# Performance work log

Hardware: AMD Instinct MI355X
Metric: run time of the kernel (lower is better)

## Reference

```python
import jax, jax.numpy as jnp
import numpy as np
import math

B, T, D = 2, 2048, 1024
H, HKV = 16, 4
HD = D // H            # 64
G = H // HKV           # GQA group size = 4
ROPE_BASE = 10000.0


def _rope(x, cos, sin):
    # x: [B, T, h, HD]; rotate-half rotary embedding
    half = x.shape[-1] // 2
    x1, x2 = x[..., :half], x[..., half:]
    c = cos[None, :, None, :]  # [1,T,1,HD/2]
    s = sin[None, :, None, :]
    return jnp.concatenate([x1 * c - x2 * s, x1 * s + x2 * c], axis=-1)


def setup_inputs() -> dict:
    key = jax.random.key(0)
    ks = jax.random.split(key, 6)
    sD = 1.0 / math.sqrt(D)
    x = jax.random.normal(ks[0], (B, T, D), dtype=jnp.float32)
    Wq = jax.random.normal(ks[1], (D, D), dtype=jnp.float32) * sD
    Wk = jax.random.normal(ks[2], (HKV * HD, D), dtype=jnp.float32) * sD
    Wv = jax.random.normal(ks[3], (HKV * HD, D), dtype=jnp.float32) * sD
    Wp = jax.random.normal(ks[4], (D, D), dtype=jnp.float32) * sD
    q_gain = jnp.full((H,), 0.125, dtype=jnp.float32)  # qk_gain_init
    return {"x": x, "Wq": Wq, "Wk": Wk, "Wv": Wv, "Wp": Wp, "q_gain": q_gain}


def reference(x, Wq, Wk, Wv, Wp, q_gain):
    Bx, Tx, _ = x.shape
    # QKV projections (CastedLinear == plain no-bias linear in fp32 here)
    q = (x @ Wq.T).reshape(Bx, Tx, H, HD)
    k = (x @ Wk.T).reshape(Bx, Tx, HKV, HD)
    v = (x @ Wv.T).reshape(Bx, Tx, HKV, HD)

    # rotary tables
    inv_freq = 1.0 / (ROPE_BASE ** (jnp.arange(0, HD, 2, dtype=jnp.float32) / HD))
    freqs = jnp.arange(Tx, dtype=jnp.float32)[:, None] * inv_freq[None, :]  # [T, HD/2]
    cos, sin = jnp.cos(freqs), jnp.sin(freqs)

    q = _rope(q, cos, sin) * q_gain[None, None, :, None]  # per-head learned gain
    k = _rope(k, cos, sin)

    # grouped-query causal attention
    qg = q.reshape(Bx, Tx, HKV, G, HD)
    scale = 1.0 / math.sqrt(HD)
    scores = jnp.einsum('bqkgd,bskd->bkgqs', qg, k) * scale  # [B,HKV,G,T,T]
    causal = jnp.tril(jnp.ones((Tx, Tx), dtype=bool))
    scores = jnp.where(causal[None, None, None], scores, jnp.float32(-1e30))
    p = jax.nn.softmax(scores, axis=-1)
    o = jnp.einsum('bkgqs,bskd->bqkgd', p, v).reshape(Bx, Tx, D)
    return o @ Wp.T
```

## Files before the change

### kernel.cpp

```cpp
#include <hip/hip_runtime.h>

typedef unsigned short u16;
typedef unsigned int   u32;
typedef __bf16 bfv8 __attribute__((ext_vector_type(8)));
typedef float  f32x4 __attribute__((ext_vector_type(4)));
typedef short  s16x4 __attribute__((ext_vector_type(4)));

#define B_   2
#define T_   2048
#define D_   1024
#define H_   16
#define HKV_ 4
#define NQK  1280
#define BT_  (B_*T_)
#define QSCALE 0.18033688011112042f
#define L2_10K 0.41524101186092515f
#define I2PI   0.15915494309189535f

__device__ __forceinline__ u16 f2bf(float f) {
  __bf16 h = (__bf16)f; u16 s; __builtin_memcpy(&s, &h, 2); return s;
}

__device__ __forceinline__ void load16(const u16* g, u16* l) {
  auto gp = (const __attribute__((address_space(1))) u32*)(uintptr_t)g;
  auto lp = (__attribute__((address_space(3))) u32*)(uintptr_t)l;
  __builtin_amdgcn_global_load_lds(gp, lp, 16, 0, 0);
}

__device__ __forceinline__ void hw_sincos_rev(float rev, float& s, float& c) {
  rev -= floorf(rev);
  s = __builtin_amdgcn_sinf(rev);
  c = __builtin_amdgcn_cosf(rev);
}

__global__ void conv_all_kernel(const float* __restrict__ x,
                                const float* __restrict__ wq, const float* __restrict__ wk,
                                const float* __restrict__ wv, const float* __restrict__ wp,
                                u16* __restrict__ dst) {
  int i = (blockIdx.x * 256 + threadIdx.x) * 4;
  const float* s; int off;
  if (i < 4194304) { s = x; off = i; }
  else {
    int j = i - 4194304;
    if      (j < 1048576) { s = wq; off = j; }
    else if (j < 1310720) { s = wk; off = j - 1048576; }
    else if (j < 1572864) { s = wv; off = j - 1310720; }
    else                  { s = wp; off = j - 1572864; }
  }
  float4 v = *(const float4*)(s + off);
  ushort4 o; o.x = f2bf(v.x); o.y = f2bf(v.y); o.z = f2bf(v.z); o.w = f2bf(v.w);
  *(ushort4*)(dst + i) = o;
}

template<int MODE>
__global__ __launch_bounds__(256) void gemm_bt(const u16* __restrict__ A,
                                               const u16* __restrict__ Bm,
                                               void* __restrict__ C,
                                               u16* __restrict__ vT,
                                               const float* __restrict__ qg,
                                               int M, int N, int K) {
  __shared__ __align__(16) u16 As[2][128 * 32];
  __shared__ __align__(16) u16 Bs[2][128 * 32];
  const int tid  = threadIdx.x;
  const int wave = tid >> 6, lane = tid & 63;
  const int quad = lane >> 4, l16 = lane & 15;
  const int m0 = blockIdx.y * 128, n0 = blockIdx.x * 128;
  const int wm = (wave >> 1) * 64, wn = (wave & 1) * 64;
  const int lr = lane >> 2, lc = (lane & 3) * 8;

  f32x4 acc[4][4];
  for (int mi = 0; mi < 4; ++mi)
    for (int ni = 0; ni < 4; ++ni) acc[mi][ni] = (f32x4){0.f, 0.f, 0.f, 0.f};

  auto stage = [&](int kk, int buf) {
    #pragma unroll
    for (int u = 0; u < 2; ++u) {
      const int c = u * 4 + wave;
      load16(A + (size_t)(m0 + c*16 + lr) * K + kk + lc, As[buf] + c * 512);
    }
    #pragma unroll
    for (int u = 0; u < 2; ++u) {
      const int c = u * 4 + wave;
      load16(Bm + (size_t)(n0 + c*16 + lr) * K + kk + lc, Bs[buf] + c * 512);
    }
  };

  const int nIter = K >> 5;
  stage(0, 0);
  for (int it = 0; it < nIter; ++it) {
    __syncthreads();
    if (it + 1 < nIter) stage(((it + 1) << 5), (it + 1) & 1);
    const u16* Ab = As[it & 1];
    const u16* Bb = Bs[it & 1];
    bfv8 af[4], bf_[4];
    #pragma unroll
    for (int i = 0; i < 4; ++i) af[i]  = *(const bfv8*)(Ab + (wm + i*16 + l16)*32 + 8*quad);
    #pragma unroll
    for (int i = 0; i < 4; ++i) bf_[i] = *(const bfv8*)(Bb + (wn + i*16 + l16)*32 + 8*quad);
    #pragma unroll
    for (int mi = 0; mi < 4; ++mi)
      #pragma unroll
      for (int ni = 0; ni < 4; ++ni)
        acc[mi][ni] = __builtin_amdgcn_mfma_f32_16x16x32_bf16(af[mi], bf_[ni], acc[mi][ni], 0, 0, 0);
  }

  const int nc = n0 + wn;
  if (MODE == 0) {
    #pragma unroll
    for (int mi = 0; mi < 4; ++mi)
      #pragma unroll
      for (int ni = 0; ni < 4; ++ni)
        #pragma unroll
        for (int r = 0; r < 4; ++r)
          ((float*)C)[(size_t)(m0 + wm + mi*16 + 4*quad + r) * N + nc + ni*16 + l16]
            = acc[mi][ni][r];
  } else {
    if (nc < NQK) {
      const bool isQ = nc < 1024;
      const float gain = isQ ? qg[nc >> 6] * QSCALE : 1.0f;
      const float inv0 = exp2f(-(float)l16 * L2_10K) * I2PI;
      const float inv1 = exp2f(-(float)(l16 + 16) * L2_10K) * I2PI;
      #pragma unroll
      for (int mi = 0; mi < 4; ++mi) {
        const int rowg = m0 + wm + mi*16 + 4*quad;
        u16* dst = (u16*)C + (size_t)rowg * NQK + nc + l16;
        #pragma unroll
        for (int r = 0; r < 4; ++r) {
          const int t = (rowg + r) & (T_ - 1);
          float s0, c0, s1, c1;
          hw_sincos_rev((float)t * inv0, s0, c0);
          hw_sincos_rev((float)t * inv1, s1, c1);
          const float x1a = acc[mi][0][r], x2a = acc[mi][2][r];
          const float x1b = acc[mi][1][r], x2b = acc[mi][3][r];
          u16* drow = dst + (size_t)r * NQK;
          drow[0]  = f2bf((x1a*c0 - x2a*s0) * gain);
          drow[16] = f2bf((x1b*c1 - x2b*s1) * gain);
          drow[32] = f2bf((x1a*s0 + x2a*c0) * gain);
          drow[48] = f2bf((x1b*s1 + x2b*c1) * gain);
        }
      }
    } else {
      const int kvh = (nc - NQK) >> 6;
      #pragma unroll
      for (int mi = 0; mi < 4; ++mi)
        #pragma unroll
        for (int ni = 0; ni < 4; ++ni) {
          const int d = ni*16 + l16;
          const int rowg = m0 + wm + mi*16 + 4*quad;
          const int bb = rowg >> 11, t = rowg & (T_ - 1);
          ushort4 w4;
          w4.x = f2bf(acc[mi][ni][0]); w4.y = f2bf(acc[mi][ni][1]);
          w4.z = f2bf(acc[mi][ni][2]); w4.w = f2bf(acc[mi][ni][3]);
          *(ushort4*)(vT + ((size_t)((bb*HKV_ + kvh)*64 + d)) * T_ + t) = w4;
        }
    }
  }
}

template<bool DOA, bool DIAGA, bool DIAGB>
__device__ __forceinline__ void attn_tile(const u16* KB, const u16* VB,
                                          int l16, int quad,
                                          const bfv8* qA, const bfv8* qB,
                                          float& psA, float& psB,
                                          f32x4 oA[4], f32x4 oB[4],
                                          int qColA, int qColB, int s0) {
  const int sw = l16 & 7;
  f32x4 stA[4], stB[4];
  #pragma unroll
  for (int ni = 0; ni < 4; ++ni) {
    const int row = ni*16 + l16;
    bfv8 k0 = *(const bfv8*)(KB + row*64 + 8*(quad ^ sw));
    bfv8 k1 = *(const bfv8*)(KB + row*64 + 8*((quad + 4) ^ sw));
    if (DOA) {
      stA[ni] = __builtin_amdgcn_mfma_f32_16x16x32_bf16(k0, qA[0], (f32x4){0.f,0.f,0.f,0.f}, 0, 0, 0);
      stA[ni] = __builtin_amdgcn_mfma_f32_16x16x32_bf16(k1, qA[1], stA[ni], 0, 0, 0);
    }
    stB[ni] = __builtin_amdgcn_mfma_f32_16x16x32_bf16(k0, qB[0], (f32x4){0.f,0.f,0.f,0.f}, 0, 0, 0);
    stB[ni] = __builtin_amdgcn_mfma_f32_16x16x32_bf16(k1, qB[1], stB[ni], 0, 0, 0);
  }
  s16x4 pbA[4], pbB[4];
  #pragma unroll
  for (int ni = 0; ni < 4; ++ni)
    #pragma unroll
    for (int r = 0; r < 4; ++r) {
      const int key = s0 + ni*16 + 4*quad + r;
      if (DOA) {
        float v = stA[ni][r];
        if (DIAGA) v = (key <= qColA) ? v : -3.0e38f;
        const float p = __builtin_amdgcn_exp2f(v);
        psA += p;
        pbA[ni][r] = (short)f2bf(p);
      }
      float v = stB[ni][r];
      if (DIAGB) v = (key <= qColB) ? v : -3.0e38f;
      const float p = __builtin_amdgcn_exp2f(v);
      psB += p;
      pbB[ni][r] = (short)f2bf(p);
    }
  #pragma unroll
  for (int ni = 0; ni < 4; ++ni) {
    const int vofs = 8*((2*ni + (quad >> 1)) ^ sw) + 4*(quad & 1);
    #pragma unroll
    for (int dt = 0; dt < 4; ++dt) {
      s16x4 va = *(const s16x4*)(VB + (dt*16 + l16)*64 + vofs);
      if (DOA) oA[dt] = __builtin_amdgcn_mfma_f32_16x16x16bf16_1k(va, pbA[ni], oA[dt], 0, 0, 0);
      oB[dt] = __builtin_amdgcn_mfma_f32_16x16x16bf16_1k(va, pbB[ni], oB[dt], 0, 0, 0);
    }
  }
}

__global__ __launch_bounds__(256) void attn_kernel(const u16* __restrict__ qkv,
                                                   const u16* __restrict__ vT,
                                                   u16* __restrict__ o) {
  const int pr = blockIdx.x;
  const int h  = blockIdx.y;
  const int b  = blockIdx.z;
  const int kvh = h >> 2;
  const int tid = threadIdx.x;
  const int wave = tid >> 6, lane = tid & 63;
  const int quad = lane >> 4, l16 = lane & 15;

  const int qtA = pr, qtB = 31 - pr;
  const int nk  = qtB + 1;

  __shared__ __align__(16) u16 Kl[2][64 * 64];
  __shared__ __align__(16) u16 Vl[2][64 * 64];

  const u16* qAp = qkv + (size_t)(b*T_ + qtA*64 + wave*16 + l16) * NQK + h*64 + 8*quad;
  const u16* qBp = qkv + (size_t)(b*T_ + qtB*64 + wave*16 + l16) * NQK + h*64 + 8*quad;
  const bfv8 qA[2] = { *(const bfv8*)qAp, *(const bfv8*)(qAp + 32) };
  const bfv8 qB[2] = { *(const bfv8*)qBp, *(const bfv8*)(qBp + 32) };

  float psA = 0.f, psB = 0.f;
  f32x4 oA[4], oB[4];
  #pragma unroll
  for (int d = 0; d < 4; ++d) oA[d] = oB[d] = (f32x4){0.f, 0.f, 0.f, 0.f};

  const int srow = lane >> 3, slot = lane & 7;
  const u16* Kg = qkv + (size_t)(b*T_) * NQK + 1024 + kvh*64;
  const u16* Vg = vT  + (size_t)((b*HKV_ + kvh) * 64) * T_;

  auto stage = [&](int kt, int buf) {
    const int s0 = kt * 64;
    #pragma unroll
    for (int u = 0; u < 2; ++u) {
      const int base = wave*16 + u*8;
      const int r  = base + srow;
      const int kc = slot ^ (r & 7);
      load16(Kg + (size_t)(s0 + r) * NQK + kc*8, Kl[buf] + base*64);
      load16(Vg + (size_t)r * T_ + s0 + kc*8,    Vl[buf] + base*64);
    }
  };

  stage(0, 0);
  const int qColA = qtA*64 + wave*16 + l16;
  const int qColB = qtB*64 + wave*16 + l16;

  for (int kt = 0; kt < qtA; ++kt) {
    __syncthreads();
    stage(kt + 1, (kt + 1) & 1);
    attn_tile<true, false, false>(Kl[kt & 1], Vl[kt & 1], l16, quad, qA, qB,
                                  psA, psB, oA, oB, qColA, qColB, kt*64);
  }
  {
    const int kt = qtA;
    __syncthreads();
    stage(kt + 1, (kt + 1) & 1);
    attn_tile<true, true, false>(Kl[kt & 1], Vl[kt & 1], l16, quad, qA, qB,
                                 psA, psB, oA, oB, qColA, qColB, kt*64);
  }
  for (int kt = qtA + 1; kt < nk - 1; ++kt) {
    __syncthreads();
    stage(kt + 1, (kt + 1) & 1);
    attn_tile<false, false, false>(Kl[kt & 1], Vl[kt & 1], l16, quad, qA, qB,
                                   psA, psB, oA, oB, qColA, qColB, kt*64);
  }
  {
    const int kt = nk - 1;
    __syncthreads();
    attn_tile<false, false, true>(Kl[kt & 1], Vl[kt & 1], l16, quad, qA, qB,
                                  psA, psB, oA, oB, qColA, qColB, kt*64);
  }

  #pragma unroll
  for (int off = 16; off < 64; off <<= 1) {
    psA += __shfl_xor(psA, off);
    psB += __shfl_xor(psB, off);
  }
  const float ivA = 1.0f / psA, ivB = 1.0f / psB;

  #pragma unroll
  for (int dt = 0; dt < 4; ++dt) {
    ushort4 wA, wB;
    wA.x = f2bf(oA[dt][0]*ivA); wA.y = f2bf(oA[dt][1]*ivA);
    wA.z = f2bf(oA[dt][2]*ivA); wA.w = f2bf(oA[dt][3]*ivA);
    wB.x = f2bf(oB[dt][0]*ivB); wB.y = f2bf(oB[dt][1]*ivB);
    wB.z = f2bf(oB[dt][2]*ivB); wB.w = f2bf(oB[dt][3]*ivB);
    *(ushort4*)(o + (size_t)(b*T_ + qColA) * D_ + h*64 + dt*16 + 4*quad) = wA;
    *(ushort4*)(o + (size_t)(b*T_ + qColB) * D_ + h*64 + dt*16 + 4*quad) = wB;
  }
}

extern "C" void kernel_launch(void* const* d_in, const int* in_sizes, int n_in,
                              void* d_out, int out_size, void* d_ws, size_t ws_size,
                              hipStream_t stream) {
  const float* x  = (const float*)d_in[0];
  const float* Wq = (const float*)d_in[1];
  const float* Wk = (const float*)d_in[2];
  const float* Wv = (const float*)d_in[3];
  const float* Wp = (const float*)d_in[4];
  const float* qg = (const float*)d_in[5];

  u16* xb   = (u16*)d_ws;
  u16* wqkv = xb   + (size_t)BT_ * D_;
  u16* wpb  = wqkv + (size_t)1536 * D_;
  u16* qkvb = wpb  + (size_t)D_ * D_;
  u16* vT   = qkvb + (size_t)BT_ * NQK;
  u16* ob   = xb;

  conv_all_kernel<<<dim3((4194304 + 2621440) / 1024), dim3(256), 0, stream>>>(
      x, Wq, Wk, Wv, Wp, xb);

  gemm_bt<2><<<dim3(12, 32), dim3(256), 0, stream>>>(xb, wqkv, qkvb, vT, qg, BT_, 1536, D_);
  attn_kernel<<<dim3(16, H_, B_), dim3(256), 0, stream>>>(qkvb, vT, ob);
  gemm_bt<0><<<dim3(8, 32), dim3(256), 0, stream>>>(ob, wpb, d_out, (u16*)nullptr, nullptr, BT_, D_, D_);
}
```

Measured before the change: 157.6 us.

## Deepen GEMM and attention pipelines to 4-buffer with vmcnt waits; shrink GEMM tiles

Both GEMMs and the attention kernel move from a double-buffered __syncthreads loop to a 4-slot LDS ring with prefetch distance two. Each step waits only on its own loads using s_waitcnt vmcnt plus s_barrier, so the next tile's global loads stay in flight during compute. The GEMM also changes to 64x128 tiles with 128 threads, which doubles the block count and gives more blocks in flight for these M sizes. The risks are higher LDS use per block, which can lower occupancy, and reuse of a ring slot while other waves may still be reading it, since the wait sits after the next stage is issued.

```diff
diff --git a/kernel.cpp b/kernel.cpp
--- a/kernel.cpp
+++ b/kernel.cpp
@@ -16,6 +16,8 @@
 #define QSCALE 0.18033688011112042f
 #define L2_10K 0.41524101186092515f
 #define I2PI   0.15915494309189535f
+
+#define WAITBAR(N) asm volatile("s_waitcnt vmcnt(" #N ")\n\ts_barrier" ::: "memory")
 
 __device__ __forceinline__ u16 f2bf(float f) {
   __bf16 h = (__bf16)f; u16 s; __builtin_memcpy(&s, &h, 2); return s;
@@ -53,19 +55,19 @@
 }
 
 template<int MODE>
-__global__ __launch_bounds__(256) void gemm_bt(const u16* __restrict__ A,
+__global__ __launch_bounds__(128) void gemm_bt(const u16* __restrict__ A,
                                                const u16* __restrict__ Bm,
                                                void* __restrict__ C,
                                                u16* __restrict__ vT,
                                                const float* __restrict__ qg,
                                                int M, int N, int K) {
-  __shared__ __align__(16) u16 As[2][128 * 32];
-  __shared__ __align__(16) u16 Bs[2][128 * 32];
+  __shared__ __align__(16) u16 As[4][64 * 32];
+  __shared__ __align__(16) u16 Bs[4][128 * 32];
   const int tid  = threadIdx.x;
   const int wave = tid >> 6, lane = tid & 63;
   const int quad = lane >> 4, l16 = lane & 15;
-  const int m0 = blockIdx.y * 128, n0 = blockIdx.x * 128;
-  const int wm = (wave >> 1) * 64, wn = (wave & 1) * 64;
+  const int m0 = blockIdx.y * 64, n0 = blockIdx.x * 128;
+  const int wn = wave * 64;
   const int lr = lane >> 2, lc = (lane & 3) * 8;
 
   f32x4 acc[4][4];
@@ -75,26 +77,22 @@
   auto stage = [&](int kk, int buf) {
     #pragma unroll
     for (int u = 0; u < 2; ++u) {
-      const int c = u * 4 + wave;
+      const int c = u * 2 + wave;
       load16(A + (size_t)(m0 + c*16 + lr) * K + kk + lc, As[buf] + c * 512);
     }
     #pragma unroll
-    for (int u = 0; u < 2; ++u) {
-      const int c = u * 4 + wave;
+    for (int u = 0; u < 4; ++u) {
+      const int c = u * 2 + wave;
       load16(Bm + (size_t)(n0 + c*16 + lr) * K + kk + lc, Bs[buf] + c * 512);
     }
   };
 
-  const int nIter = K >> 5;
-  stage(0, 0);
-  for (int it = 0; it < nIter; ++it) {
-    __syncthreads();
-    if (it + 1 < nIter) stage(((it + 1) << 5), (it + 1) & 1);
-    const u16* Ab = As[it & 1];
-    const u16* Bb = Bs[it & 1];
+  auto comp = [&](int it) {
+    const u16* Ab = As[it & 3];
+    const u16* Bb = Bs[it & 3];
     bfv8 af[4], bf_[4];
     #pragma unroll
-    for (int i = 0; i < 4; ++i) af[i]  = *(const bfv8*)(Ab + (wm + i*16 + l16)*32 + 8*quad);
+    for (int i = 0; i < 4; ++i) af[i]  = *(const bfv8*)(Ab + (i*16 + l16)*32 + 8*quad);
     #pragma unroll
     for (int i = 0; i < 4; ++i) bf_[i] = *(const bfv8*)(Bb + (wn + i*16 + l16)*32 + 8*quad);
     #pragma unroll
@@ -102,7 +100,20 @@
       #pragma unroll
       for (int ni = 0; ni < 4; ++ni)
         acc[mi][ni] = __builtin_amdgcn_mfma_f32_16x16x32_bf16(af[mi], bf_[ni], acc[mi][ni], 0, 0, 0);
-  }
+  };
+
+  const int nIter = K >> 5;
+  stage(0, 0);
+  stage(32, 1);
+  for (int it = 0; it < nIter - 2; ++it) {
+    stage((it + 2) << 5, (it + 2) & 3);
+    WAITBAR(12);
+    comp(it);
+  }
+  WAITBAR(6);
+  comp(nIter - 2);
+  WAITBAR(0);
+  comp(nIter - 1);
 
   const int nc = n0 + wn;
   if (MODE == 0) {
@@ -112,7 +123,7 @@
       for (int ni = 0; ni < 4; ++ni)
         #pragma unroll
         for (int r = 0; r < 4; ++r)
-          ((float*)C)[(size_t)(m0 + wm + mi*16 + 4*quad + r) * N + nc + ni*16 + l16]
+          ((float*)C)[(size_t)(m0 + mi*16 + 4*quad + r) * N + nc + ni*16 + l16]
             = acc[mi][ni][r];
   } else {
     if (nc < NQK) {
@@ -122,7 +133,7 @@
       const float inv1 = exp2f(-(float)(l16 + 16) * L2_10K) * I2PI;
       #pragma unroll
       for (int mi = 0; mi < 4; ++mi) {
-        const int rowg = m0 + wm + mi*16 + 4*quad;
+        const int rowg = m0 + mi*16 + 4*quad;
         u16* dst = (u16*)C + (size_t)rowg * NQK + nc + l16;
         #pragma unroll
         for (int r = 0; r < 4; ++r) {
@@ -146,7 +157,7 @@
         #pragma unroll
         for (int ni = 0; ni < 4; ++ni) {
           const int d = ni*16 + l16;
-          const int rowg = m0 + wm + mi*16 + 4*quad;
+          const int rowg = m0 + mi*16 + 4*quad;
           const int bb = rowg >> 11, t = rowg & (T_ - 1);
           ushort4 w4;
           w4.x = f2bf(acc[mi][ni][0]); w4.y = f2bf(acc[mi][ni][1]);
@@ -223,8 +234,8 @@
   const int qtA = pr, qtB = 31 - pr;
   const int nk  = qtB + 1;
 
-  __shared__ __align__(16) u16 Kl[2][64 * 64];
-  __shared__ __align__(16) u16 Vl[2][64 * 64];
+  __shared__ __align__(16) u16 Kl[4][64 * 64];
+  __shared__ __align__(16) u16 Vl[4][64 * 64];
 
   const u16* qAp = qkv + (size_t)(b*T_ + qtA*64 + wave*16 + l16) * NQK + h*64 + 8*quad;
   const u16* qBp = qkv + (size_t)(b*T_ + qtB*64 + wave*16 + l16) * NQK + h*64 + 8*quad;
@@ -252,33 +263,37 @@
     }
   };
 
+  auto pipe = [&](int kt) {
+    if (kt + 2 < nk) { stage(kt + 2, (kt + 2) & 3); WAITBAR(8); }
+    else if (kt + 1 < nk) { WAITBAR(4); }
+    else { WAITBAR(0); }
+  };
+
   stage(0, 0);
+  stage(1, 1);
   const int qColA = qtA*64 + wave*16 + l16;
   const int qColB = qtB*64 + wave*16 + l16;
 
   for (int kt = 0; kt < qtA; ++kt) {
-    __syncthreads();
-    stage(kt + 1, (kt + 1) & 1);
-    attn_tile<true, false, false>(Kl[kt & 1], Vl[kt & 1], l16, quad, qA, qB,
+    pipe(kt);
+    attn_tile<true, false, false>(Kl[kt & 3], Vl[kt & 3], l16, quad, qA, qB,
                                   psA, psB, oA, oB, qColA, qColB, kt*64);
   }
   {
     const int kt = qtA;
-    __syncthreads();
-    stage(kt + 1, (kt + 1) & 1);
-    attn_tile<true, true, false>(Kl[kt & 1], Vl[kt & 1], l16, quad, qA, qB,
+    pipe(kt);
+    attn_tile<true, true, false>(Kl[kt & 3], Vl[kt & 3], l16, quad, qA, qB,
                                  psA, psB, oA, oB, qColA, qColB, kt*64);
   }
   for (int kt = qtA + 1; kt < nk - 1; ++kt) {
-    __syncthreads();
-    stage(kt + 1, (kt + 1) & 1);
-    attn_tile<false, false, false>(Kl[kt & 1], Vl[kt & 1], l16, quad, qA, qB,
+    pipe(kt);
+    attn_tile<false, false, false>(Kl[kt & 3], Vl[kt & 3], l16, quad, qA, qB,
                                    psA, psB, oA, oB, qColA, qColB, kt*64);
   }
   {
     const int kt = nk - 1;
-    __syncthreads();
-    attn_tile<false, false, true>(Kl[kt & 1], Vl[kt & 1], l16, quad, qA, qB,
+    pipe(kt);
+    attn_tile<false, false, true>(Kl[kt & 3], Vl[kt & 3], l16, quad, qA, qB,
                                   psA, psB, oA, oB, qColA, qColB, kt*64);
   }
 
@@ -321,7 +336,7 @@
   conv_all_kernel<<<dim3((4194304 + 2621440) / 1024), dim3(256), 0, stream>>>(
       x, Wq, Wk, Wv, Wp, xb);
 
-  gemm_bt<2><<<dim3(12, 32), dim3(256), 0, stream>>>(xb, wqkv, qkvb, vT, qg, BT_, 1536, D_);
+  gemm_bt<2><<<dim3(12, 64), dim3(128), 0, stream>>>(xb, wqkv, qkvb, vT, qg, BT_, 1536, D_);
   attn_kernel<<<dim3(16, H_, B_), dim3(256), 0, stream>>>(qkvb, vT, ob);
-  gemm_bt<0><<<dim3(8, 32), dim3(256), 0, stream>>>(ob, wpb, d_out, (u16*)nullptr, nullptr, BT_, D_, D_);
-}
+  gemm_bt<0><<<dim3(8, 64), dim3(128), 0, stream>>>(ob, wpb, d_out, (u16*)nullptr, nullptr, BT_, D_, D_);
+}
```

Result: slower. 162.1 us (+2.9%).

## Load K and V tiles directly from global memory into registers, dropping LDS staging

Applied to the files above, without the earlier changes.

Removes the double-buffered shared-memory staging of K and V tiles and the per-tile __syncthreads. Each wave now reads its MFMA operand fragments for K and transposed V straight from global memory (L2-cached) into registers at the start of each tile. This cuts LDS traffic and block-level synchronisation but loses the async prefetch overlap. Every wave now re-reads the same K/V data from global or L2, and load latency is exposed unless the compiler hoists the loads.

```diff
diff --git a/kernel.cpp b/kernel.cpp
--- a/kernel.cpp
+++ b/kernel.cpp
@@ -158,25 +158,37 @@
 }
 
 template<bool DOA, bool DIAGA, bool DIAGB>
-__device__ __forceinline__ void attn_tile(const u16* KB, const u16* VB,
+__device__ __forceinline__ void attn_tile(const u16* __restrict__ Kg,
+                                          const u16* __restrict__ Vg,
                                           int l16, int quad,
                                           const bfv8* qA, const bfv8* qB,
                                           float& psA, float& psB,
                                           f32x4 oA[4], f32x4 oB[4],
                                           int qColA, int qColB, int s0) {
-  const int sw = l16 & 7;
+  bfv8 k0[4], k1[4];
+  s16x4 va[4][4];
+  #pragma unroll
+  for (int ni = 0; ni < 4; ++ni) {
+    const u16* Krow = Kg + (size_t)(s0 + ni*16 + l16) * NQK + 8*quad;
+    k0[ni] = *(const bfv8*)(Krow);
+    k1[ni] = *(const bfv8*)(Krow + 32);
+  }
+  #pragma unroll
+  for (int dt = 0; dt < 4; ++dt) {
+    const u16* Vrow = Vg + (size_t)(dt*16 + l16) * T_ + s0 + 4*quad;
+    #pragma unroll
+    for (int ni = 0; ni < 4; ++ni)
+      va[dt][ni] = *(const s16x4*)(Vrow + 16*ni);
+  }
   f32x4 stA[4], stB[4];
   #pragma unroll
   for (int ni = 0; ni < 4; ++ni) {
-    const int row = ni*16 + l16;
-    bfv8 k0 = *(const bfv8*)(KB + row*64 + 8*(quad ^ sw));
-    bfv8 k1 = *(const bfv8*)(KB + row*64 + 8*((quad + 4) ^ sw));
     if (DOA) {
-      stA[ni] = __builtin_amdgcn_mfma_f32_16x16x32_bf16(k0, qA[0], (f32x4){0.f,0.f,0.f,0.f}, 0, 0, 0);
-      stA[ni] = __builtin_amdgcn_mfma_f32_16x16x32_bf16(k1, qA[1], stA[ni], 0, 0, 0);
-    }
-    stB[ni] = __builtin_amdgcn_mfma_f32_16x16x32_bf16(k0, qB[0], (f32x4){0.f,0.f,0.f,0.f}, 0, 0, 0);
-    stB[ni] = __builtin_amdgcn_mfma_f32_16x16x32_bf16(k1, qB[1], stB[ni], 0, 0, 0);
+      stA[ni] = __builtin_amdgcn_mfma_f32_16x16x32_bf16(k0[ni], qA[0], (f32x4){0.f,0.f,0.f,0.f}, 0, 0, 0);
+      stA[ni] = __builtin_amdgcn_mfma_f32_16x16x32_bf16(k1[ni], qA[1], stA[ni], 0, 0, 0);
+    }
+    stB[ni] = __builtin_amdgcn_mfma_f32_16x16x32_bf16(k0[ni], qB[0], (f32x4){0.f,0.f,0.f,0.f}, 0, 0, 0);
+    stB[ni] = __builtin_amdgcn_mfma_f32_16x16x32_bf16(k1[ni], qB[1], stB[ni], 0, 0, 0);
   }
   s16x4 pbA[4], pbB[4];
   #pragma unroll
@@ -198,15 +210,12 @@
       pbB[ni][r] = (short)f2bf(p);
     }
   #pragma unroll
-  for (int ni = 0; ni < 4; ++ni) {
-    const int vofs = 8*((2*ni + (quad >> 1)) ^ sw) + 4*(quad & 1);
+  for (int ni = 0; ni < 4; ++ni)
     #pragma unroll
     for (int dt = 0; dt < 4; ++dt) {
-      s16x4 va = *(const s16x4*)(VB + (dt*16 + l16)*64 + vofs);
-      if (DOA) oA[dt] = __builtin_amdgcn_mfma_f32_16x16x16bf16_1k(va, pbA[ni], oA[dt], 0, 0, 0);
-      oB[dt] = __builtin_amdgcn_mfma_f32_16x16x16bf16_1k(va, pbB[ni], oB[dt], 0, 0, 0);
-    }
-  }
+      if (DOA) oA[dt] = __builtin_amdgcn_mfma_f32_16x16x16bf16_1k(va[dt][ni], pbA[ni], oA[dt], 0, 0, 0);
+      oB[dt] = __builtin_amdgcn_mfma_f32_16x16x16bf16_1k(va[dt][ni], pbB[ni], oB[dt], 0, 0, 0);
+    }
 }
 
 __global__ __launch_bounds__(256) void attn_kernel(const u16* __restrict__ qkv,
@@ -223,9 +232,6 @@
   const int qtA = pr, qtB = 31 - pr;
   const int nk  = qtB + 1;
 
-  __shared__ __align__(16) u16 Kl[2][64 * 64];
-  __shared__ __align__(16) u16 Vl[2][64 * 64];
-
   const u16* qAp = qkv + (size_t)(b*T_ + qtA*64 + wave*16 + l16) * NQK + h*64 + 8*quad;
   const u16* qBp = qkv + (size_t)(b*T_ + qtB*64 + wave*16 + l16) * NQK + h*64 + 8*quad;
   const bfv8 qA[2] = { *(const bfv8*)qAp, *(const bfv8*)(qAp + 32) };
@@ -236,51 +242,22 @@
   #pragma unroll
   for (int d = 0; d < 4; ++d) oA[d] = oB[d] = (f32x4){0.f, 0.f, 0.f, 0.f};
 
-  const int srow = lane >> 3, slot = lane & 7;
   const u16* Kg = qkv + (size_t)(b*T_) * NQK + 1024 + kvh*64;
   const u16* Vg = vT  + (size_t)((b*HKV_ + kvh) * 64) * T_;
 
-  auto stage = [&](int kt, int buf) {
-    const int s0 = kt * 64;
-    #pragma unroll
-    for (int u = 0; u < 2; ++u) {
-      const int base = wave*16 + u*8;
-      const int r  = base + srow;
-      const int kc = slot ^ (r & 7);
-      load16(Kg + (size_t)(s0 + r) * NQK + kc*8, Kl[buf] + base*64);
-      load16(Vg + (size_t)r * T_ + s0 + kc*8,    Vl[buf] + base*64);
-    }
-  };
-
-  stage(0, 0);
   const int qColA = qtA*64 + wave*16 + l16;
   const int qColB = qtB*64 + wave*16 + l16;
 
-  for (int kt = 0; kt < qtA; ++kt) {
-    __syncthreads();
-    stage(kt + 1, (kt + 1) & 1);
-    attn_tile<true, false, false>(Kl[kt & 1], Vl[kt & 1], l16, quad, qA, qB,
+  for (int kt = 0; kt < qtA; ++kt)
+    attn_tile<true, false, false>(Kg, Vg, l16, quad, qA, qB,
                                   psA, psB, oA, oB, qColA, qColB, kt*64);
-  }
-  {
-    const int kt = qtA;
-    __syncthreads();
-    stage(kt + 1, (kt + 1) & 1);
-    attn_tile<true, true, false>(Kl[kt & 1], Vl[kt & 1], l16, quad, qA, qB,
-                                 psA, psB, oA, oB, qColA, qColB, kt*64);
-  }
-  for (int kt = qtA + 1; kt < nk - 1; ++kt) {
-    __syncthreads();
-    stage(kt + 1, (kt + 1) & 1);
-    attn_tile<false, false, false>(Kl[kt & 1], Vl[kt & 1], l16, quad, qA, qB,
+  attn_tile<true, true, false>(Kg, Vg, l16, quad, qA, qB,
+                               psA, psB, oA, oB, qColA, qColB, qtA*64);
+  for (int kt = qtA + 1; kt < nk - 1; ++kt)
+    attn_tile<false, false, false>(Kg, Vg, l16, quad, qA, qB,
                                    psA, psB, oA, oB, qColA, qColB, kt*64);
-  }
-  {
-    const int kt = nk - 1;
-    __syncthreads();
-    attn_tile<false, false, true>(Kl[kt & 1], Vl[kt & 1], l16, quad, qA, qB,
-                                  psA, psB, oA, oB, qColA, qColB, kt*64);
-  }
+  attn_tile<false, false, true>(Kg, Vg, l16, quad, qA, qB,
+                                psA, psB, oA, oB, qColA, qColB, (nk-1)*64);
 
   #pragma unroll
   for (int off = 16; off < 64; off <<= 1) {
```

After: 295.2 us. 1.87x slower.
